# Performance work log

Measured on AMD Instinct MI355X. Metric: run time of the kernel, lower is better.

The kernel has to match this reference:

```python
import jax, jax.numpy as jnp
import numpy as np

NUM_EXPERTS = 8
TOP_K = 2
LORA_ALPHA = 2.0
LORA_RANK = 16
D_MODEL = 2048
D_HIDDEN = 5632


def setup_inputs() -> dict:
    key = jax.random.key(0)
    ks = jax.random.split(key, 11)
    B, S, D, H, E, R = 2, 1024, D_MODEL, D_HIDDEN, NUM_EXPERTS, LORA_RANK
    sd = 1.0 / np.sqrt(D)
    sh = 1.0 / np.sqrt(H)
    x = jax.random.normal(ks[0], (B, S, D), jnp.float32)
    gate_w = jax.random.normal(ks[1], (E, D), jnp.float32) * sd   # router Linear(D->E), no bias
    w_up = jax.random.normal(ks[2], (H, D), jnp.float32) * sd     # up_proj.weight
    w_gate = jax.random.normal(ks[3], (H, D), jnp.float32) * sd   # gate_proj.weight
    w_down = jax.random.normal(ks[4], (D, H), jnp.float32) * sh   # down_proj.weight
    up_A = jax.random.normal(ks[5], (E, R, D), jnp.float32) * sd
    up_B = jax.random.normal(ks[6], (E, H, R), jnp.float32) * 0.02
    gate_A = jax.random.normal(ks[7], (E, R, D), jnp.float32) * sd
    gate_B = jax.random.normal(ks[8], (E, H, R), jnp.float32) * 0.02
    down_A = jax.random.normal(ks[9], (E, R, H), jnp.float32) * sh
    down_B = jax.random.normal(ks[10], (E, D, R), jnp.float32) * 0.02
    return {"x": x, "gate_w": gate_w, "w_up": w_up, "w_gate": w_gate,
            "w_down": w_down, "up_A": up_A, "up_B": up_B,
            "gate_A": gate_A, "gate_B": gate_B, "down_A": down_A, "down_B": down_B}


def reference(x, gate_w, w_up, w_gate, w_down, up_A, up_B, gate_A, gate_B, down_A, down_B):
    B, S, D = x.shape
    H = w_up.shape[0]
    # router: logits [B,S,E], top-k over experts (last dim)
    gate_logits = jnp.einsum('bsd,ed->bse', x, gate_w)
    topw, sel = jax.lax.top_k(gate_logits, TOP_K)            # [B,S,k]
    # NOTE: source applies softmax over dim=1 (the SEQUENCE axis) -- reproduced faithfully
    topw = jax.nn.softmax(topw.astype(jnp.float32), axis=1).astype(x.dtype)
    xt = x.reshape(-1, D)                                    # [T, D]
    wf = topw.reshape(-1, TOP_K)                             # [T, k]
    sf = sel.reshape(-1, TOP_K)                              # [T, k]
    # shared base projections computed once for all tokens
    base_up = xt @ w_up.T                                    # [T, H]
    base_gate = xt @ w_gate.T                                # [T, H]
    mixed_h = jnp.zeros((xt.shape[0], H), x.dtype)
    lora_down = jnp.zeros_like(xt)
    # loop over fixed small expert count; low-rank LoRA deltas applied without
    # materializing full merged weights (same math by linearity of matmul)
    for e in range(NUM_EXPERTS):
        c = jnp.sum(jnp.where(sf == e, wf, 0.0), axis=1)     # [T] routing weight (0 if not routed)
        lo_up = LORA_ALPHA * ((xt @ up_A[e].T) @ up_B[e].T)
        lo_gate = LORA_ALPHA * ((xt @ gate_A[e].T) @ gate_B[e].T)
        h_e = jax.nn.silu(base_up + lo_up) * (base_gate + lo_gate)  # [T, H]
        ch = c[:, None] * h_e
        mixed_h = mixed_h + ch
        lora_down = lora_down + LORA_ALPHA * ((ch @ down_A[e].T) @ down_B[e].T)
    out = mixed_h @ w_down.T + lora_down                     # base down GEMM done once on mixed hidden
    return out.reshape(B, S, D)
```

## Files before the change

kernel.cpp:

```cpp
#include <hip/hip_runtime.h>
#include <hip/hip_fp16.h>
#include <cmath>

#define TOKENS 2048
#define DMODEL 2048
#define DHID   5632
#define NEXP   8
#define RANK   16
#define LALPHA 2.0f

typedef __attribute__((ext_vector_type(4))) float f32x4;
typedef __attribute__((ext_vector_type(8))) short s16x8;
typedef __attribute__((ext_vector_type(4))) short s16x4;
typedef __attribute__((ext_vector_type(8))) _Float16 f16x8;

__device__ __forceinline__ short f2bf(float f){
  unsigned u = __float_as_uint(f);
  u += 0x7fffu + ((u >> 16) & 1u);
  return (short)(u >> 16);
}

struct Stage { const short* s0; const short* s1; short* d0; short* d1; };

__device__ __forceinline__ Stage mk_stage(const short* g, long ld, short* t, int tid){
  Stage st;
  const int L0 = tid,      r0 = L0>>2, c0 = ((L0&3) - (r0>>1)) & 3;
  const int L1 = 256+tid,  r1 = L1>>2, c1 = ((L1&3) - (r1>>1)) & 3;
  st.s0 = g + (long)r0*ld + c0*8;  st.d0 = t + L0*8;
  st.s1 = g + (long)r1*ld + c1*8;  st.d1 = t + L1*8;
  return st;
}
__device__ __forceinline__ void do_stage(const Stage& st, int k0){
  __builtin_amdgcn_global_load_lds((const __attribute__((address_space(1))) void*)(st.s0 + k0),
                                   (__attribute__((address_space(3))) void*)st.d0, 16, 0, 0);
  __builtin_amdgcn_global_load_lds((const __attribute__((address_space(1))) void*)(st.s1 + k0),
                                   (__attribute__((address_space(3))) void*)st.d1, 16, 0, 0);
}
__device__ __forceinline__ s16x8 fragb(const short* t, int row, int quad){
  const int p = (quad + (row>>1)) & 3;
  return *(const s16x8*)(t + (row*4 + p)*8);
}
__device__ __forceinline__ f16x8 fragh(const short* t, int row, int quad){
  const int p = (quad + (row>>1)) & 3;
  return *(const f16x8*)(t + (row*4 + p)*8);
}

__global__ void k_cast(const float* __restrict__ x, const float* __restrict__ w_up,
                       const float* __restrict__ w_gate, const float* __restrict__ w_down,
                       const float* __restrict__ upA, const float* __restrict__ gateA,
                       const float* __restrict__ downA, const float* __restrict__ upB,
                       const float* __restrict__ gateB, const float* __restrict__ downB,
                       short* __restrict__ xb, short* __restrict__ wub, short* __restrict__ wgb,
                       short* __restrict__ wdb, short* __restrict__ acat, short* __restrict__ daA,
                       short* __restrict__ upBh, short* __restrict__ gateBh, short* __restrict__ wdbcat){
  const long e0 = 4194304, e1 = 15728640, e2 = 27262976, e3 = 38797312;
  const long e4 = 39518208, e5 = 40239104, e6 = 40960000, e7 = 41484288, e8 = 41746432;
  const long i = ((long)blockIdx.x*256 + threadIdx.x) * 4;
  if(i >= e8) return;
  const float* src; short* dst; long l; int fp16 = 0;
  if(i < e0){ src = x; dst = xb; l = i; }
  else if(i < e1){ src = w_up; dst = wub; l = i - e0; }
  else if(i < e2){ src = w_gate; dst = wgb; l = i - e1; }
  else if(i < e3){ src = w_down; dst = wdb; l = i - e2; }
  else if(i < e4){ src = downA; dst = daA; l = i - e3; }
  else if(i < e5){ src = upB; dst = upBh; l = i - e4; fp16 = 1; }
  else if(i < e6){ src = gateB; dst = gateBh; l = i - e5; fp16 = 1; }
  else if(i < e7){
    l = i - e6;
    const long c = l>>11, d = l&2047;
    const long e = c>>5, pj = (c>>4)&1, r = c&15;
    src = (pj ? gateA : upA) + ((e*RANK + r)<<11) + d - l;
    dst = acat;
  } else {
    l = i - e7;
    const long d = l>>7, c = l&127;
    const long e = c>>4, r = c&15;
    src = downB + (e*DMODEL + d)*RANK + r - l;
    dst = wdbcat; fp16 = 1;
  }
  const float4 v = *(const float4*)(src + l);
  s16x4 o;
  if(fp16){
    o[0]=(short)__half_as_ushort(__float2half(v.x));
    o[1]=(short)__half_as_ushort(__float2half(v.y));
    o[2]=(short)__half_as_ushort(__float2half(v.z));
    o[3]=(short)__half_as_ushort(__float2half(v.w));
  } else {
    o[0]=f2bf(v.x); o[1]=f2bf(v.y); o[2]=f2bf(v.z); o[3]=f2bf(v.w);
  }
  *(s16x4*)(dst + l) = o;
}

__global__ void k_router(const float* __restrict__ x, const float* __restrict__ gw,
                         int* __restrict__ sel, float* __restrict__ topv){
  const int t = blockIdx.x*4 + (threadIdx.x>>6);
  const int lane = threadIdx.x & 63;
  const float* xr = x + (long)t * DMODEL;
  float acc[NEXP];
  #pragma unroll
  for(int e=0;e<NEXP;e++) acc[e]=0.f;
  #pragma unroll
  for(int it=0; it<8; it++){
    const int d = it*256 + lane*4;
    const float4 xv = *(const float4*)(xr + d);
    #pragma unroll
    for(int e=0;e<NEXP;e++){
      const float4 wv = *(const float4*)(gw + e*DMODEL + d);
      acc[e] += xv.x*wv.x + xv.y*wv.y + xv.z*wv.z + xv.w*wv.w;
    }
  }
  #pragma unroll
  for(int e=0;e<NEXP;e++){
    #pragma unroll
    for(int off=32; off; off>>=1) acc[e] += __shfl_down(acc[e], off, 64);
  }
  if(lane==0){
    int i0=0;
    #pragma unroll
    for(int e=1;e<NEXP;e++) if(acc[e]>acc[i0]) i0=e;
    int i1=-1;
    #pragma unroll
    for(int e=0;e<NEXP;e++){ if(e==i0) continue; if(i1<0 || acc[e]>acc[i1]) i1=e; }
    sel[t*2+0]=i0; sel[t*2+1]=i1;
    topv[t*2+0]=acc[i0]; topv[t*2+1]=acc[i1];
  }
}

__global__ void k_softmax(const float* __restrict__ topv, float* __restrict__ cw){
  const int b = blockIdx.x >> 1, k = blockIdx.x & 1;
  const int base = b*1024;
  __shared__ float red[256];
  float v[4];
  float mx = -1e30f;
  #pragma unroll
  for(int i=0;i<4;i++){
    int s = threadIdx.x + i*256;
    v[i] = topv[(base+s)*2 + k];
    mx = fmaxf(mx, v[i]);
  }
  red[threadIdx.x]=mx; __syncthreads();
  for(int o=128;o;o>>=1){ if(threadIdx.x<o) red[threadIdx.x]=fmaxf(red[threadIdx.x],red[threadIdx.x+o]); __syncthreads(); }
  mx = red[0]; __syncthreads();
  float sum=0.f;
  #pragma unroll
  for(int i=0;i<4;i++){ v[i]=__expf(v[i]-mx); sum+=v[i]; }
  red[threadIdx.x]=sum; __syncthreads();
  for(int o=128;o;o>>=1){ if(threadIdx.x<o) red[threadIdx.x]+=red[threadIdx.x+o]; __syncthreads(); }
  const float inv = 1.f/red[0];
  #pragma unroll
  for(int i=0;i<4;i++){
    int s = threadIdx.x + i*256;
    cw[(base+s)*2+k] = v[i]*inv;
  }
}

__global__ __launch_bounds__(256,3) void k_rank(
    const short* __restrict__ xb, const short* __restrict__ acat, float* __restrict__ Rall){
  __shared__ __align__(16) short At[4096];
  __shared__ __align__(16) short Bt[4096];
  const int c0 = blockIdx.x*128, t0 = blockIdx.y*128;
  const int tid = threadIdx.x, lane = tid&63, wave = tid>>6;
  const int wm=(wave>>1)*64, wn=(wave&1)*64, fr=lane&15, quad=lane>>4;
  f32x4 acc[4][4];
  #pragma unroll
  for(int i=0;i<4;i++)
    #pragma unroll
    for(int j=0;j<4;j++) acc[i][j]=(f32x4){0.f,0.f,0.f,0.f};
  const Stage sA = mk_stage(xb + (long)t0*DMODEL, DMODEL, At, tid);
  const Stage sB = mk_stage(acat + (long)c0*DMODEL, DMODEL, Bt, tid);
  for(int k0=0; k0<DMODEL; k0+=32){
    do_stage(sA, k0); do_stage(sB, k0);
    __syncthreads();
    s16x8 af[4];
    #pragma unroll
    for(int i=0;i<4;i++) af[i] = fragb(At, wm + i*16 + fr, quad);
    #pragma unroll
    for(int j=0;j<4;j++){
      const s16x8 bf = fragb(Bt, wn + j*16 + fr, quad);
      #pragma unroll
      for(int i=0;i<4;i++)
        acc[i][j] = __builtin_amdgcn_mfma_f32_16x16x32_bf16(af[i], bf, acc[i][j], 0,0,0);
    }
    __syncthreads();
  }
  #pragma unroll
  for(int i=0;i<4;i++)
    #pragma unroll
    for(int j=0;j<4;j++){
      const int rbase = wm + i*16 + quad*4, col = wn + j*16 + fr;
      #pragma unroll
      for(int reg=0;reg<4;reg++)
        Rall[(long)(t0+rbase+reg)*256 + c0 + col] = acc[i][j][reg];
    }
}

struct K4Smem {
  union {
    struct { short A[4096]; short U[4096]; short G[4096]; } st;
    struct { __half rub[128][2][32]; float cwv[128][2]; int sele[128][2]; } ep;
  } u;
};

__global__ __launch_bounds__(256,2) void k_main(
    const short* __restrict__ xb, const short* __restrict__ wub, const short* __restrict__ wgb,
    const __half* __restrict__ upBh, const __half* __restrict__ gateBh,
    const float* __restrict__ Rall, const int* __restrict__ sel, const float* __restrict__ cw,
    unsigned short* __restrict__ ch){
  __shared__ __align__(16) K4Smem sm;
  const int h0 = blockIdx.x*128, t0 = blockIdx.y*128;
  const int tid = threadIdx.x, lane = tid&63, wave = tid>>6;
  const int wm=(wave>>1)*64, wn=(wave&1)*64, fr=lane&15, quad=lane>>4;
  f32x4 au[4][4], ag[4][4];
  #pragma unroll
  for(int i=0;i<4;i++)
    #pragma unroll
    for(int j=0;j<4;j++){ au[i][j]=(f32x4){0.f,0.f,0.f,0.f}; ag[i][j]=(f32x4){0.f,0.f,0.f,0.f}; }
  const Stage sA = mk_stage(xb + (long)t0*DMODEL, DMODEL, sm.u.st.A, tid);
  const Stage sU = mk_stage(wub + (long)h0*DMODEL, DMODEL, sm.u.st.U, tid);
  const Stage sG = mk_stage(wgb + (long)h0*DMODEL, DMODEL, sm.u.st.G, tid);
  for(int k0=0; k0<DMODEL; k0+=32){
    do_stage(sA, k0); do_stage(sU, k0); do_stage(sG, k0);
    __syncthreads();
    s16x8 af[4];
    #pragma unroll
    for(int i=0;i<4;i++) af[i] = fragb(sm.u.st.A, wm + i*16 + fr, quad);
    #pragma unroll
    for(int j=0;j<4;j++){
      const s16x8 bu = fragb(sm.u.st.U, wn + j*16 + fr, quad);
      const s16x8 bg = fragb(sm.u.st.G, wn + j*16 + fr, quad);
      #pragma unroll
      for(int i=0;i<4;i++){
        au[i][j] = __builtin_amdgcn_mfma_f32_16x16x32_bf16(af[i], bu, au[i][j], 0,0,0);
        ag[i][j] = __builtin_amdgcn_mfma_f32_16x16x32_bf16(af[i], bg, ag[i][j], 0,0,0);
      }
    }
    __syncthreads();
  }
  for(int i2 = tid; i2 < 256; i2 += 256){
    const int tl = i2>>1, k = i2&1;
    sm.u.ep.sele[tl][k] = sel[(t0+tl)*2 + k];
    sm.u.ep.cwv[tl][k]  = cw[(t0+tl)*2 + k];
  }
  for(int i2 = tid; i2 < 128*2*32; i2 += 256){
    const int tl = i2>>6, k = (i2>>5)&1, r = i2&31;
    const int e = sel[(t0+tl)*2 + k];
    sm.u.ep.rub[tl][k][r] = __float2half(LALPHA * Rall[(long)(t0+tl)*256 + e*32 + r]);
  }
  __syncthreads();
  #pragma unroll
  for(int i=0;i<4;i++){
    #pragma unroll
    for(int reg=0;reg<4;reg++){
      const int tl = wm + i*16 + quad*4 + reg;
      #pragma unroll
      for(int k=0;k<2;k++){
        const int e = sm.u.ep.sele[tl][k];
        const float c = sm.u.ep.cwv[tl][k];
        __half2 rv[16];
        #pragma unroll
        for(int q=0;q<4;q++) *(s16x8*)&rv[q*4] = *(const s16x8*)&sm.u.ep.rub[tl][k][q*8];
        const __half* ubase = upBh   + (long)e*DHID*RANK;
        const __half* gbase = gateBh + (long)e*DHID*RANK;
        unsigned short* chrow = ch + ((long)k*TOKENS + t0+tl)*DHID + h0;
        #pragma unroll
        for(int j=0;j<4;j++){
          const int hl = wn + j*16 + fr;
          const __half2* ub = (const __half2*)(ubase + (long)(h0+hl)*RANK);
          const __half2* gb = (const __half2*)(gbase + (long)(h0+hl)*RANK);
          __half2 a2 = __half2{__half(0.f),__half(0.f)}, b2 = a2;
          #pragma unroll
          for(int r=0;r<8;r++){ a2 = __hfma2(rv[r], ub[r], a2); b2 = __hfma2(rv[8+r], gb[r], b2); }
          const float lu = __low2float(a2) + __high2float(a2);
          const float lg = __low2float(b2) + __high2float(b2);
          const float uu = au[i][j][reg] + lu;
          const float gg = ag[i][j][reg] + lg;
          const float hv = (uu / (1.f + __expf(-uu))) * gg;
          chrow[hl] = (unsigned short)f2bf(c * hv);
        }
      }
    }
  }
}

__global__ __launch_bounds__(256,3) void k_rd(
    const unsigned short* __restrict__ ch, const short* __restrict__ daA,
    float* __restrict__ RD){
  __shared__ __align__(16) short At[4096];
  __shared__ __align__(16) short Bt[4096];
  const int slot = blockIdx.x>>3, ks = blockIdx.x&7;
  const int t0 = blockIdx.y*128;
  const int tid = threadIdx.x, lane = tid&63, wave = tid>>6;
  const int wm=(wave>>1)*64, wn=(wave&1)*64, fr=lane&15, quad=lane>>4;
  f32x4 acc[4][4];
  #pragma unroll
  for(int i=0;i<4;i++)
    #pragma unroll
    for(int j=0;j<4;j++) acc[i][j]=(f32x4){0.f,0.f,0.f,0.f};
  const Stage sA = mk_stage((const short*)ch + ((long)slot*TOKENS + t0)*DHID, DHID, At, tid);
  const Stage sB = mk_stage(daA, DHID, Bt, tid);
  const int kbeg = ks*704;
  for(int kk=0; kk<704; kk+=32){
    do_stage(sA, kbeg+kk); do_stage(sB, kbeg+kk);
    __syncthreads();
    s16x8 af[4];
    #pragma unroll
    for(int i=0;i<4;i++) af[i] = fragb(At, wm + i*16 + fr, quad);
    #pragma unroll
    for(int j=0;j<4;j++){
      const s16x8 bf = fragb(Bt, wn + j*16 + fr, quad);
      #pragma unroll
      for(int i=0;i<4;i++)
        acc[i][j] = __builtin_amdgcn_mfma_f32_16x16x32_bf16(af[i], bf, acc[i][j], 0,0,0);
    }
    __syncthreads();
  }
  #pragma unroll
  for(int i=0;i<4;i++)
    #pragma unroll
    for(int j=0;j<4;j++){
      const int rbase = wm + i*16 + quad*4, col = wn + j*16 + fr;
      #pragma unroll
      for(int reg=0;reg<4;reg++)
        atomicAdd(&RD[((long)(t0+rbase+reg)*2 + slot)*128 + col], acc[i][j][reg]);
    }
}

__global__ void k_scatter(const float* __restrict__ RD, const int* __restrict__ sel,
                          __half* __restrict__ RDhat){
  const int idx = blockIdx.x*256 + threadIdx.x;
  const int t = idx>>7, c = idx&127, e = c>>4;
  const int s0 = sel[t*2], s1 = sel[t*2+1];
  float v = 0.f;
  if(e == s0) v = LALPHA * RD[((long)t*2+0)*128 + c];
  else if(e == s1) v = LALPHA * RD[((long)t*2+1)*128 + c];
  RDhat[idx] = __float2half(v);
}

__global__ __launch_bounds__(256,3) void k_down(
    const unsigned short* __restrict__ ch, const short* __restrict__ wdb,
    const short* __restrict__ RDhat, const short* __restrict__ wdbcat,
    float* __restrict__ out){
  __shared__ __align__(16) short A0t[4096];
  __shared__ __align__(16) short A1t[4096];
  __shared__ __align__(16) short Bt[4096];
  const int d0 = blockIdx.x*128, t0 = blockIdx.y*128;
  const int tid = threadIdx.x, lane = tid&63, wave = tid>>6;
  const int wm=(wave>>1)*64, wn=(wave&1)*64, fr=lane&15, quad=lane>>4;
  f32x4 acc[4][4];
  #pragma unroll
  for(int i=0;i<4;i++)
    #pragma unroll
    for(int j=0;j<4;j++) acc[i][j]=(f32x4){0.f,0.f,0.f,0.f};
  const Stage sA0 = mk_stage((const short*)ch + (long)t0*DHID, DHID, A0t, tid);
  const Stage sA1 = mk_stage((const short*)ch + ((long)TOKENS + t0)*DHID, DHID, A1t, tid);
  const Stage sB  = mk_stage(wdb + (long)d0*DHID, DHID, Bt, tid);
  for(int k0=0; k0<DHID; k0+=32){
    do_stage(sA0, k0); do_stage(sA1, k0); do_stage(sB, k0);
    __syncthreads();
    s16x8 a0[4], a1[4];
    #pragma unroll
    for(int i=0;i<4;i++){ a0[i] = fragb(A0t, wm + i*16 + fr, quad); a1[i] = fragb(A1t, wm + i*16 + fr, quad); }
    #pragma unroll
    for(int j=0;j<4;j++){
      const s16x8 bf = fragb(Bt, wn + j*16 + fr, quad);
      #pragma unroll
      for(int i=0;i<4;i++){
        acc[i][j] = __builtin_amdgcn_mfma_f32_16x16x32_bf16(a0[i], bf, acc[i][j], 0,0,0);
        acc[i][j] = __builtin_amdgcn_mfma_f32_16x16x32_bf16(a1[i], bf, acc[i][j], 0,0,0);
      }
    }
    __syncthreads();
  }
  const Stage sAh = mk_stage(RDhat + (long)t0*128, 128, A0t, tid);
  const Stage sBh = mk_stage(wdbcat + (long)d0*128, 128, Bt, tid);
  for(int k0=0; k0<128; k0+=32){
    do_stage(sAh, k0); do_stage(sBh, k0);
    __syncthreads();
    f16x8 af[4];
    #pragma unroll
    for(int i=0;i<4;i++) af[i] = fragh(A0t, wm + i*16 + fr, quad);
    #pragma unroll
    for(int j=0;j<4;j++){
      const f16x8 bf = fragh(Bt, wn + j*16 + fr, quad);
      #pragma unroll
      for(int i=0;i<4;i++)
        acc[i][j] = __builtin_amdgcn_mfma_f32_16x16x32_f16(af[i], bf, acc[i][j], 0,0,0);
    }
    __syncthreads();
  }
  #pragma unroll
  for(int i=0;i<4;i++)
    #pragma unroll
    for(int j=0;j<4;j++){
      const int rbase = wm + i*16 + quad*4, col = wn + j*16 + fr;
      #pragma unroll
      for(int reg=0;reg<4;reg++)
        out[(long)(t0+rbase+reg)*DMODEL + d0 + col] = acc[i][j][reg];
    }
}

extern "C" void kernel_launch(void* const* d_in, const int* in_sizes, int n_in,
                              void* d_out, int out_size, void* d_ws, size_t ws_size,
                              hipStream_t stream){
  (void)in_sizes; (void)n_in; (void)out_size; (void)ws_size;
  const float* x      = (const float*)d_in[0];
  const float* gate_w = (const float*)d_in[1];
  const float* w_up   = (const float*)d_in[2];
  const float* w_gate = (const float*)d_in[3];
  const float* w_down = (const float*)d_in[4];
  const float* up_A   = (const float*)d_in[5];
  const float* up_B   = (const float*)d_in[6];
  const float* gate_A = (const float*)d_in[7];
  const float* gate_B = (const float*)d_in[8];
  const float* down_A = (const float*)d_in[9];
  const float* down_B = (const float*)d_in[10];
  float* out = (float*)d_out;

  char* ws = (char*)d_ws;
  size_t off = 0;
  auto alloc = [&](size_t bytes){ void* p = ws + off; off += (bytes + 255) & ~(size_t)255; return p; };
  short* xb     = (short*)alloc((size_t)TOKENS*DMODEL*2);
  short* wub    = (short*)alloc((size_t)DHID*DMODEL*2);
  short* wgb    = (short*)alloc((size_t)DHID*DMODEL*2);
  short* wdb    = (short*)alloc((size_t)DMODEL*DHID*2);
  short* acat   = (short*)alloc((size_t)256*DMODEL*2);
  short* daA    = (short*)alloc((size_t)128*DHID*2);
  short* upBh   = (short*)alloc((size_t)NEXP*DHID*RANK*2);
  short* gateBh = (short*)alloc((size_t)NEXP*DHID*RANK*2);
  short* wdbcat = (short*)alloc((size_t)DMODEL*128*2);
  unsigned short* ch = (unsigned short*)alloc((size_t)2*TOKENS*DHID*2);
  float* Rall   = (float*)alloc((size_t)TOKENS*256*4);
  float* RD     = (float*)alloc((size_t)TOKENS*2*128*4);
  __half* RDhat = (__half*)alloc((size_t)TOKENS*128*2);
  int*   sel    = (int*)alloc((size_t)TOKENS*2*4);
  float* topv   = (float*)alloc((size_t)TOKENS*2*4);
  float* cw     = (float*)alloc((size_t)TOKENS*2*4);

  (void)hipMemsetAsync(RD, 0, (size_t)TOKENS*2*128*4, stream);
  k_cast<<<40768, 256, 0, stream>>>(x, w_up, w_gate, w_down, up_A, gate_A, down_A,
                                    up_B, gate_B, down_B,
                                    xb, wub, wgb, wdb, acat, daA, upBh, gateBh, wdbcat);
  k_router<<<512, 256, 0, stream>>>(x, gate_w, sel, topv);
  k_softmax<<<4, 256, 0, stream>>>(topv, cw);
  k_rank<<<dim3(2,16), 256, 0, stream>>>(xb, acat, Rall);
  k_main<<<dim3(44,16), 256, 0, stream>>>(xb, wub, wgb, (const __half*)upBh, (const __half*)gateBh, Rall, sel, cw, ch);
  k_rd<<<dim3(16,16), 256, 0, stream>>>(ch, daA, RD);
  k_scatter<<<1024, 256, 0, stream>>>(RD, sel, RDhat);
  k_down<<<dim3(16,16), 256, 0, stream>>>(ch, wdb, (const short*)RDhat, wdbcat, out);
}
```

Baseline: 611.8 us.

## Move LoRA-B expansion to MFMA, pre-sum hidden slots, split-K down GEMM

The LoRA up/gate B-projection in k_main now runs as fp16 MFMA GEMMs. They read a new masked per-expert rank activation buffer built by k_rsel, replacing the per-element half2 FMA epilogue with gathered B rows. k_main also writes a pre-summed hidden tensor, so the down GEMM streams one A operand instead of two. The down GEMM is split along K into two slices that combine with atomicAdd into a zero-initialised output, and k_rd's K-split is doubled. In exchange it adds extra MFMA work over masked zeros and much higher register pressure from six accumulator sets under launch bounds of 3, plus atomics and an extra memset.

```diff
diff --git a/kernel.cpp b/kernel.cpp
--- a/kernel.cpp
+++ b/kernel.cpp
@@ -18,6 +18,9 @@
   unsigned u = __float_as_uint(f);
   u += 0x7fffu + ((u >> 16) & 1u);
   return (short)(u >> 16);
+}
+__device__ __forceinline__ short f2h(float f){
+  return (short)__half_as_ushort(__float2half(f));
 }
 
 struct Stage { const short* s0; const short* s1; short* d0; short* d1; };
@@ -51,10 +54,10 @@
                        const float* __restrict__ downA, const float* __restrict__ upB,
                        const float* __restrict__ gateB, const float* __restrict__ downB,
                        short* __restrict__ xb, short* __restrict__ wub, short* __restrict__ wgb,
-                       short* __restrict__ wdb, short* __restrict__ acat, short* __restrict__ daA,
-                       short* __restrict__ upBh, short* __restrict__ gateBh, short* __restrict__ wdbcat){
+                       short* __restrict__ wdb, short* __restrict__ daA, short* __restrict__ acat,
+                       short* __restrict__ upBcat, short* __restrict__ gateBcat, short* __restrict__ wdbcat){
   const long e0 = 4194304, e1 = 15728640, e2 = 27262976, e3 = 38797312;
-  const long e4 = 39518208, e5 = 40239104, e6 = 40960000, e7 = 41484288, e8 = 41746432;
+  const long e4 = 39518208, e5 = 40042496, e6 = 40763392, e7 = 41484288, e8 = 41746432;
   const long i = ((long)blockIdx.x*256 + threadIdx.x) * 4;
   if(i >= e8) return;
   const float* src; short* dst; long l; int fp16 = 0;
@@ -63,31 +66,35 @@
   else if(i < e2){ src = w_gate; dst = wgb; l = i - e1; }
   else if(i < e3){ src = w_down; dst = wdb; l = i - e2; }
   else if(i < e4){ src = downA; dst = daA; l = i - e3; }
-  else if(i < e5){ src = upB; dst = upBh; l = i - e4; fp16 = 1; }
-  else if(i < e6){ src = gateB; dst = gateBh; l = i - e5; fp16 = 1; }
+  else if(i < e5){
+    l = i - e4;
+    const long c = l>>11;
+    const long e = c>>5, pj = (c>>4)&1, r = c&15;
+    src = (pj ? gateA : upA) + ((e*RANK + r)<<11) + (l&2047) - l;
+    dst = acat;
+  }
+  else if(i < e6){
+    l = i - e5;
+    const long h = l>>7, c = l&127, e = c>>4, r = c&15;
+    src = upB + ((e*DHID + h)*RANK + r) - l;
+    dst = upBcat; fp16 = 1;
+  }
   else if(i < e7){
     l = i - e6;
-    const long c = l>>11, d = l&2047;
-    const long e = c>>5, pj = (c>>4)&1, r = c&15;
-    src = (pj ? gateA : upA) + ((e*RANK + r)<<11) + d - l;
-    dst = acat;
-  } else {
+    const long h = l>>7, c = l&127, e = c>>4, r = c&15;
+    src = gateB + ((e*DHID + h)*RANK + r) - l;
+    dst = gateBcat; fp16 = 1;
+  }
+  else {
     l = i - e7;
-    const long d = l>>7, c = l&127;
-    const long e = c>>4, r = c&15;
-    src = downB + (e*DMODEL + d)*RANK + r - l;
+    const long d = l>>7, c = l&127, e = c>>4, r = c&15;
+    src = downB + ((e*DMODEL + d)*RANK + r) - l;
     dst = wdbcat; fp16 = 1;
   }
   const float4 v = *(const float4*)(src + l);
   s16x4 o;
-  if(fp16){
-    o[0]=(short)__half_as_ushort(__float2half(v.x));
-    o[1]=(short)__half_as_ushort(__float2half(v.y));
-    o[2]=(short)__half_as_ushort(__float2half(v.z));
-    o[3]=(short)__half_as_ushort(__float2half(v.w));
-  } else {
-    o[0]=f2bf(v.x); o[1]=f2bf(v.y); o[2]=f2bf(v.z); o[3]=f2bf(v.w);
-  }
+  if(fp16){ o[0]=f2h(v.x); o[1]=f2h(v.y); o[2]=f2h(v.z); o[3]=f2h(v.w); }
+  else    { o[0]=f2bf(v.x); o[1]=f2bf(v.y); o[2]=f2bf(v.z); o[3]=f2bf(v.w); }
   *(s16x4*)(dst + l) = o;
 }
 
@@ -194,100 +201,138 @@
     }
 }
 
-struct K4Smem {
-  union {
-    struct { short A[4096]; short U[4096]; short G[4096]; } st;
-    struct { __half rub[128][2][32]; float cwv[128][2]; int sele[128][2]; } ep;
-  } u;
-};
-
-__global__ __launch_bounds__(256,2) void k_main(
+__global__ void k_rsel(const float* __restrict__ Rall, const int* __restrict__ sel,
+                       short* __restrict__ RselU, short* __restrict__ RselG){
+  const int idx = blockIdx.x*256 + threadIdx.x;
+  const int c = idx & 127, t = (idx>>7) & (TOKENS-1), k = idx>>18;
+  const int e = c>>4, r = c&15;
+  const int s = sel[t*2+k];
+  const int m = (e==s);
+  RselU[idx] = f2h(m ? LALPHA*Rall[(long)t*256 + e*32 + r]      : 0.f);
+  RselG[idx] = f2h(m ? LALPHA*Rall[(long)t*256 + e*32 + 16 + r] : 0.f);
+}
+
+__global__ __launch_bounds__(256,3) void k_main(
     const short* __restrict__ xb, const short* __restrict__ wub, const short* __restrict__ wgb,
-    const __half* __restrict__ upBh, const __half* __restrict__ gateBh,
-    const float* __restrict__ Rall, const int* __restrict__ sel, const float* __restrict__ cw,
-    unsigned short* __restrict__ ch){
-  __shared__ __align__(16) K4Smem sm;
+    const short* __restrict__ RselU, const short* __restrict__ RselG,
+    const short* __restrict__ upBcat, const short* __restrict__ gateBcat,
+    const float* __restrict__ cw, unsigned short* __restrict__ ch, unsigned short* __restrict__ chsum){
+  __shared__ __align__(16) short At[4096];
+  __shared__ __align__(16) short Ut[4096];
+  __shared__ __align__(16) short Gt[4096];
+  __shared__ float cwv[128][2];
   const int h0 = blockIdx.x*128, t0 = blockIdx.y*128;
   const int tid = threadIdx.x, lane = tid&63, wave = tid>>6;
   const int wm=(wave>>1)*64, wn=(wave&1)*64, fr=lane&15, quad=lane>>4;
-  f32x4 au[4][4], ag[4][4];
-  #pragma unroll
-  for(int i=0;i<4;i++)
-    #pragma unroll
-    for(int j=0;j<4;j++){ au[i][j]=(f32x4){0.f,0.f,0.f,0.f}; ag[i][j]=(f32x4){0.f,0.f,0.f,0.f}; }
-  const Stage sA = mk_stage(xb + (long)t0*DMODEL, DMODEL, sm.u.st.A, tid);
-  const Stage sU = mk_stage(wub + (long)h0*DMODEL, DMODEL, sm.u.st.U, tid);
-  const Stage sG = mk_stage(wgb + (long)h0*DMODEL, DMODEL, sm.u.st.G, tid);
-  for(int k0=0; k0<DMODEL; k0+=32){
-    do_stage(sA, k0); do_stage(sU, k0); do_stage(sG, k0);
-    __syncthreads();
-    s16x8 af[4];
-    #pragma unroll
-    for(int i=0;i<4;i++) af[i] = fragb(sm.u.st.A, wm + i*16 + fr, quad);
-    #pragma unroll
-    for(int j=0;j<4;j++){
-      const s16x8 bu = fragb(sm.u.st.U, wn + j*16 + fr, quad);
-      const s16x8 bg = fragb(sm.u.st.G, wn + j*16 + fr, quad);
-      #pragma unroll
-      for(int i=0;i<4;i++){
-        au[i][j] = __builtin_amdgcn_mfma_f32_16x16x32_bf16(af[i], bu, au[i][j], 0,0,0);
-        ag[i][j] = __builtin_amdgcn_mfma_f32_16x16x32_bf16(af[i], bg, ag[i][j], 0,0,0);
+  if(tid < 256){ const int tl = tid>>1, k = tid&1; cwv[tl][k] = cw[(t0+tl)*2 + k]; }
+  f32x4 au[4][4], ag[4][4], lu0[4][4], lg0[4][4], lu1[4][4], lg1[4][4];
+  #pragma unroll
+  for(int i=0;i<4;i++)
+    #pragma unroll
+    for(int j=0;j<4;j++){
+      au[i][j]=(f32x4){0.f,0.f,0.f,0.f}; ag[i][j]=au[i][j];
+      lu0[i][j]=au[i][j]; lg0[i][j]=au[i][j]; lu1[i][j]=au[i][j]; lg1[i][j]=au[i][j];
+    }
+  {
+    const Stage sA = mk_stage(xb + (long)t0*DMODEL, DMODEL, At, tid);
+    const Stage sU = mk_stage(wub + (long)h0*DMODEL, DMODEL, Ut, tid);
+    const Stage sG = mk_stage(wgb + (long)h0*DMODEL, DMODEL, Gt, tid);
+    for(int k0=0; k0<DMODEL; k0+=32){
+      do_stage(sA, k0); do_stage(sU, k0); do_stage(sG, k0);
+      __syncthreads();
+      s16x8 af[4];
+      #pragma unroll
+      for(int i=0;i<4;i++) af[i] = fragb(At, wm + i*16 + fr, quad);
+      #pragma unroll
+      for(int j=0;j<4;j++){
+        const s16x8 bu = fragb(Ut, wn + j*16 + fr, quad);
+        const s16x8 bg = fragb(Gt, wn + j*16 + fr, quad);
+        #pragma unroll
+        for(int i=0;i<4;i++){
+          au[i][j] = __builtin_amdgcn_mfma_f32_16x16x32_bf16(af[i], bu, au[i][j], 0,0,0);
+          ag[i][j] = __builtin_amdgcn_mfma_f32_16x16x32_bf16(af[i], bg, ag[i][j], 0,0,0);
+        }
       }
-    }
-    __syncthreads();
-  }
-  for(int i2 = tid; i2 < 256; i2 += 256){
-    const int tl = i2>>1, k = i2&1;
-    sm.u.ep.sele[tl][k] = sel[(t0+tl)*2 + k];
-    sm.u.ep.cwv[tl][k]  = cw[(t0+tl)*2 + k];
-  }
-  for(int i2 = tid; i2 < 128*2*32; i2 += 256){
-    const int tl = i2>>6, k = (i2>>5)&1, r = i2&31;
-    const int e = sel[(t0+tl)*2 + k];
-    sm.u.ep.rub[tl][k][r] = __float2half(LALPHA * Rall[(long)(t0+tl)*256 + e*32 + r]);
-  }
-  __syncthreads();
+      __syncthreads();
+    }
+  }
+  {
+    const Stage sB  = mk_stage(upBcat + (long)h0*128, 128, Ut, tid);
+    const Stage sR0 = mk_stage(RselU + (long)t0*128, 128, At, tid);
+    const Stage sR1 = mk_stage(RselU + ((long)TOKENS + t0)*128, 128, Gt, tid);
+    for(int k0=0; k0<128; k0+=32){
+      do_stage(sB, k0); do_stage(sR0, k0); do_stage(sR1, k0);
+      __syncthreads();
+      f16x8 a0[4], a1[4];
+      #pragma unroll
+      for(int i=0;i<4;i++){ a0[i] = fragh(At, wm + i*16 + fr, quad); a1[i] = fragh(Gt, wm + i*16 + fr, quad); }
+      #pragma unroll
+      for(int j=0;j<4;j++){
+        const f16x8 bf = fragh(Ut, wn + j*16 + fr, quad);
+        #pragma unroll
+        for(int i=0;i<4;i++){
+          lu0[i][j] = __builtin_amdgcn_mfma_f32_16x16x32_f16(a0[i], bf, lu0[i][j], 0,0,0);
+          lu1[i][j] = __builtin_amdgcn_mfma_f32_16x16x32_f16(a1[i], bf, lu1[i][j], 0,0,0);
+        }
+      }
+      __syncthreads();
+    }
+  }
+  {
+    const Stage sB  = mk_stage(gateBcat + (long)h0*128, 128, Ut, tid);
+    const Stage sR0 = mk_stage(RselG + (long)t0*128, 128, At, tid);
+    const Stage sR1 = mk_stage(RselG + ((long)TOKENS + t0)*128, 128, Gt, tid);
+    for(int k0=0; k0<128; k0+=32){
+      do_stage(sB, k0); do_stage(sR0, k0); do_stage(sR1, k0);
+      __syncthreads();
+      f16x8 a0[4], a1[4];
+      #pragma unroll
+      for(int i=0;i<4;i++){ a0[i] = fragh(At, wm + i*16 + fr, quad); a1[i] = fragh(Gt, wm + i*16 + fr, quad); }
+      #pragma unroll
+      for(int j=0;j<4;j++){
+        const f16x8 bf = fragh(Ut, wn + j*16 + fr, quad);
+        #pragma unroll
+        for(int i=0;i<4;i++){
+          lg0[i][j] = __builtin_amdgcn_mfma_f32_16x16x32_f16(a0[i], bf, lg0[i][j], 0,0,0);
+          lg1[i][j] = __builtin_amdgcn_mfma_f32_16x16x32_f16(a1[i], bf, lg1[i][j], 0,0,0);
+        }
+      }
+      __syncthreads();
+    }
+  }
   #pragma unroll
   for(int i=0;i<4;i++){
     #pragma unroll
     for(int reg=0;reg<4;reg++){
       const int tl = wm + i*16 + quad*4 + reg;
-      #pragma unroll
-      for(int k=0;k<2;k++){
-        const int e = sm.u.ep.sele[tl][k];
-        const float c = sm.u.ep.cwv[tl][k];
-        __half2 rv[16];
-        #pragma unroll
-        for(int q=0;q<4;q++) *(s16x8*)&rv[q*4] = *(const s16x8*)&sm.u.ep.rub[tl][k][q*8];
-        const __half* ubase = upBh   + (long)e*DHID*RANK;
-        const __half* gbase = gateBh + (long)e*DHID*RANK;
-        unsigned short* chrow = ch + ((long)k*TOKENS + t0+tl)*DHID + h0;
-        #pragma unroll
-        for(int j=0;j<4;j++){
-          const int hl = wn + j*16 + fr;
-          const __half2* ub = (const __half2*)(ubase + (long)(h0+hl)*RANK);
-          const __half2* gb = (const __half2*)(gbase + (long)(h0+hl)*RANK);
-          __half2 a2 = __half2{__half(0.f),__half(0.f)}, b2 = a2;
-          #pragma unroll
-          for(int r=0;r<8;r++){ a2 = __hfma2(rv[r], ub[r], a2); b2 = __hfma2(rv[8+r], gb[r], b2); }
-          const float lu = __low2float(a2) + __high2float(a2);
-          const float lg = __low2float(b2) + __high2float(b2);
-          const float uu = au[i][j][reg] + lu;
-          const float gg = ag[i][j][reg] + lg;
-          const float hv = (uu / (1.f + __expf(-uu))) * gg;
-          chrow[hl] = (unsigned short)f2bf(c * hv);
-        }
+      const float c0 = cwv[tl][0], c1 = cwv[tl][1];
+      unsigned short* r0 = ch + ((long)(t0+tl))*DHID + h0;
+      unsigned short* r1 = ch + ((long)TOKENS + t0+tl)*DHID + h0;
+      unsigned short* rs = chsum + ((long)(t0+tl))*DHID + h0;
+      #pragma unroll
+      for(int j=0;j<4;j++){
+        const int hl = wn + j*16 + fr;
+        const float u0 = au[i][j][reg] + lu0[i][j][reg];
+        const float g0 = ag[i][j][reg] + lg0[i][j][reg];
+        const float h0v = (u0 / (1.f + __expf(-u0))) * g0;
+        const float u1 = au[i][j][reg] + lu1[i][j][reg];
+        const float g1 = ag[i][j][reg] + lg1[i][j][reg];
+        const float h1v = (u1 / (1.f + __expf(-u1))) * g1;
+        const float v0 = c0*h0v, v1 = c1*h1v;
+        r0[hl] = (unsigned short)f2bf(v0);
+        r1[hl] = (unsigned short)f2bf(v1);
+        rs[hl] = (unsigned short)f2bf(v0+v1);
       }
     }
   }
 }
 
-__global__ __launch_bounds__(256,3) void k_rd(
+__global__ __launch_bounds__(256,4) void k_rd(
     const unsigned short* __restrict__ ch, const short* __restrict__ daA,
     float* __restrict__ RD){
   __shared__ __align__(16) short At[4096];
   __shared__ __align__(16) short Bt[4096];
-  const int slot = blockIdx.x>>3, ks = blockIdx.x&7;
+  const int slot = blockIdx.x>>4, ks = blockIdx.x&15;
   const int t0 = blockIdx.y*128;
   const int tid = threadIdx.x, lane = tid&63, wave = tid>>6;
   const int wm=(wave>>1)*64, wn=(wave&1)*64, fr=lane&15, quad=lane>>4;
@@ -298,8 +343,8 @@
     for(int j=0;j<4;j++) acc[i][j]=(f32x4){0.f,0.f,0.f,0.f};
   const Stage sA = mk_stage((const short*)ch + ((long)slot*TOKENS + t0)*DHID, DHID, At, tid);
   const Stage sB = mk_stage(daA, DHID, Bt, tid);
-  const int kbeg = ks*704;
-  for(int kk=0; kk<704; kk+=32){
+  const int kbeg = ks*352;
+  for(int kk=0; kk<352; kk+=32){
     do_stage(sA, kbeg+kk); do_stage(sB, kbeg+kk);
     __syncthreads();
     s16x8 af[4];
@@ -336,14 +381,13 @@
   RDhat[idx] = __float2half(v);
 }
 
-__global__ __launch_bounds__(256,3) void k_down(
-    const unsigned short* __restrict__ ch, const short* __restrict__ wdb,
+__global__ __launch_bounds__(256,4) void k_down(
+    const unsigned short* __restrict__ chsum, const short* __restrict__ wdb,
     const short* __restrict__ RDhat, const short* __restrict__ wdbcat,
     float* __restrict__ out){
-  __shared__ __align__(16) short A0t[4096];
-  __shared__ __align__(16) short A1t[4096];
+  __shared__ __align__(16) short At[4096];
   __shared__ __align__(16) short Bt[4096];
-  const int d0 = blockIdx.x*128, t0 = blockIdx.y*128;
+  const int d0 = blockIdx.x*128, t0 = blockIdx.y*128, ks = blockIdx.z;
   const int tid = threadIdx.x, lane = tid&63, wave = tid>>6;
   const int wm=(wave>>1)*64, wn=(wave&1)*64, fr=lane&15, quad=lane>>4;
   f32x4 acc[4][4];
@@ -351,42 +395,42 @@
   for(int i=0;i<4;i++)
     #pragma unroll
     for(int j=0;j<4;j++) acc[i][j]=(f32x4){0.f,0.f,0.f,0.f};
-  const Stage sA0 = mk_stage((const short*)ch + (long)t0*DHID, DHID, A0t, tid);
-  const Stage sA1 = mk_stage((const short*)ch + ((long)TOKENS + t0)*DHID, DHID, A1t, tid);
-  const Stage sB  = mk_stage(wdb + (long)d0*DHID, DHID, Bt, tid);
-  for(int k0=0; k0<DHID; k0+=32){
-    do_stage(sA0, k0); do_stage(sA1, k0); do_stage(sB, k0);
-    __syncthreads();
-    s16x8 a0[4], a1[4];
-    #pragma unroll
-    for(int i=0;i<4;i++){ a0[i] = fragb(A0t, wm + i*16 + fr, quad); a1[i] = fragb(A1t, wm + i*16 + fr, quad); }
+  const Stage sA = mk_stage((const short*)chsum + (long)t0*DHID, DHID, At, tid);
+  const Stage sB = mk_stage(wdb + (long)d0*DHID, DHID, Bt, tid);
+  const int kbeg = ks*2816;
+  for(int kk=0; kk<2816; kk+=32){
+    do_stage(sA, kbeg+kk); do_stage(sB, kbeg+kk);
+    __syncthreads();
+    s16x8 af[4];
+    #pragma unroll
+    for(int i=0;i<4;i++) af[i] = fragb(At, wm + i*16 + fr, quad);
     #pragma unroll
     for(int j=0;j<4;j++){
       const s16x8 bf = fragb(Bt, wn + j*16 + fr, quad);
       #pragma unroll
-      for(int i=0;i<4;i++){
-        acc[i][j] = __builtin_amdgcn_mfma_f32_16x16x32_bf16(a0[i], bf, acc[i][j], 0,0,0);
-        acc[i][j] = __builtin_amdgcn_mfma_f32_16x16x32_bf16(a1[i], bf, acc[i][j], 0,0,0);
+      for(int i=0;i<4;i++)
+        acc[i][j] = __builtin_amdgcn_mfma_f32_16x16x32_bf16(af[i], bf, acc[i][j], 0,0,0);
+    }
+    __syncthreads();
+  }
+  if(ks == 0){
+    const Stage sAh = mk_stage(RDhat + (long)t0*128, 128, At, tid);
+    const Stage sBh = mk_stage(wdbcat + (long)d0*128, 128, Bt, tid);
+    for(int k0=0; k0<128; k0+=32){
+      do_stage(sAh, k0); do_stage(sBh, k0);
+      __syncthreads();
+      f16x8 af[4];
+      #pragma unroll
+      for(int i=0;i<4;i++) af[i] = fragh(At, wm + i*16 + fr, quad);
+      #pragma unroll
+      for(int j=0;j<4;j++){
+        const f16x8 bf = fragh(Bt, wn + j*16 + fr, quad);
+        #pragma unroll
+        for(int i=0;i<4;i++)
+          acc[i][j] = __builtin_amdgcn_mfma_f32_16x16x32_f16(af[i], bf, acc[i][j], 0,0,0);
       }
-    }
-    __syncthreads();
-  }
-  const Stage sAh = mk_stage(RDhat + (long)t0*128, 128, A0t, tid);
-  const Stage sBh = mk_stage(wdbcat + (long)d0*128, 128, Bt, tid);
-  for(int k0=0; k0<128; k0+=32){
-    do_stage(sAh, k0); do_stage(sBh, k0);
-    __syncthreads();
-    f16x8 af[4];
-    #pragma unroll
-    for(int i=0;i<4;i++) af[i] = fragh(A0t, wm + i*16 + fr, quad);
-    #pragma unroll
-    for(int j=0;j<4;j++){
-      const f16x8 bf = fragh(Bt, wn + j*16 + fr, quad);
-      #pragma unroll
-      for(int i=0;i<4;i++)
-        acc[i][j] = __builtin_amdgcn_mfma_f32_16x16x32_f16(af[i], bf, acc[i][j], 0,0,0);
-    }
-    __syncthreads();
+      __syncthreads();
+    }
   }
   #pragma unroll
   for(int i=0;i<4;i++)
@@ -395,7 +439,7 @@
       const int rbase = wm + i*16 + quad*4, col = wn + j*16 + fr;
       #pragma unroll
       for(int reg=0;reg<4;reg++)
-        out[(long)(t0+rbase+reg)*DMODEL + d0 + col] = acc[i][j][reg];
+        atomicAdd(&out[(long)(t0+rbase+reg)*DMODEL + d0 + col], acc[i][j][reg]);
     }
 }
 
@@ -419,17 +463,20 @@
   char* ws = (char*)d_ws;
   size_t off = 0;
   auto alloc = [&](size_t bytes){ void* p = ws + off; off += (bytes + 255) & ~(size_t)255; return p; };
-  short* xb     = (short*)alloc((size_t)TOKENS*DMODEL*2);
-  short* wub    = (short*)alloc((size_t)DHID*DMODEL*2);
-  short* wgb    = (short*)alloc((size_t)DHID*DMODEL*2);
-  short* wdb    = (short*)alloc((size_t)DMODEL*DHID*2);
-  short* acat   = (short*)alloc((size_t)256*DMODEL*2);
-  short* daA    = (short*)alloc((size_t)128*DHID*2);
-  short* upBh   = (short*)alloc((size_t)NEXP*DHID*RANK*2);
-  short* gateBh = (short*)alloc((size_t)NEXP*DHID*RANK*2);
-  short* wdbcat = (short*)alloc((size_t)DMODEL*128*2);
-  unsigned short* ch = (unsigned short*)alloc((size_t)2*TOKENS*DHID*2);
+  short* xb       = (short*)alloc((size_t)TOKENS*DMODEL*2);
+  short* wub      = (short*)alloc((size_t)DHID*DMODEL*2);
+  short* wgb      = (short*)alloc((size_t)DHID*DMODEL*2);
+  short* wdb      = (short*)alloc((size_t)DMODEL*DHID*2);
+  short* daA      = (short*)alloc((size_t)128*DHID*2);
+  short* acat     = (short*)alloc((size_t)256*DMODEL*2);
+  short* upBcat   = (short*)alloc((size_t)DHID*128*2);
+  short* gateBcat = (short*)alloc((size_t)DHID*128*2);
+  short* wdbcat   = (short*)alloc((size_t)DMODEL*128*2);
+  unsigned short* ch    = (unsigned short*)alloc((size_t)2*TOKENS*DHID*2);
+  unsigned short* chsum = (unsigned short*)alloc((size_t)TOKENS*DHID*2);
   float* Rall   = (float*)alloc((size_t)TOKENS*256*4);
+  short* RselU  = (short*)alloc((size_t)2*TOKENS*128*2);
+  short* RselG  = (short*)alloc((size_t)2*TOKENS*128*2);
   float* RD     = (float*)alloc((size_t)TOKENS*2*128*4);
   __half* RDhat = (__half*)alloc((size_t)TOKENS*128*2);
   int*   sel    = (int*)alloc((size_t)TOKENS*2*4);
@@ -437,14 +484,16 @@
   float* cw     = (float*)alloc((size_t)TOKENS*2*4);
 
   (void)hipMemsetAsync(RD, 0, (size_t)TOKENS*2*128*4, stream);
+  (void)hipMemsetAsync(out, 0, (size_t)TOKENS*DMODEL*4, stream);
   k_cast<<<40768, 256, 0, stream>>>(x, w_up, w_gate, w_down, up_A, gate_A, down_A,
                                     up_B, gate_B, down_B,
-                                    xb, wub, wgb, wdb, acat, daA, upBh, gateBh, wdbcat);
+                                    xb, wub, wgb, wdb, daA, acat, upBcat, gateBcat, wdbcat);
   k_router<<<512, 256, 0, stream>>>(x, gate_w, sel, topv);
   k_softmax<<<4, 256, 0, stream>>>(topv, cw);
   k_rank<<<dim3(2,16), 256, 0, stream>>>(xb, acat, Rall);
-  k_main<<<dim3(44,16), 256, 0, stream>>>(xb, wub, wgb, (const __half*)upBh, (const __half*)gateBh, Rall, sel, cw, ch);
-  k_rd<<<dim3(16,16), 256, 0, stream>>>(ch, daA, RD);
+  k_rsel<<<2048, 256, 0, stream>>>(Rall, sel, RselU, RselG);
+  k_main<<<dim3(44,16), 256, 0, stream>>>(xb, wub, wgb, RselU, RselG, upBcat, gateBcat, cw, ch, chsum);
+  k_rd<<<dim3(32,16), 256, 0, stream>>>(ch, daA, RD);
   k_scatter<<<1024, 256, 0, stream>>>(RD, sel, RDhat);
-  k_down<<<dim3(16,16), 256, 0, stream>>>(ch, wdb, (const short*)RDhat, wdbcat, out);
-}
+  k_down<<<dim3(16,16,2), 256, 0, stream>>>(chsum, wdb, (const short*)RDhat, wdbcat, out);
+}
```

After: 1.289 ms. 2.11x slower.
